# Kernel tuning notes

Hardware: AMD Instinct MI355X
Metric: run time of the kernel (lower is better)

## Reference

```python
import jax, jax.numpy as jnp
import numpy as np

N_LAYERS = 2
D_MODEL = 1024
EXPAND = 2
D_INNER = EXPAND * D_MODEL   # 2048
D_STATE = 16
D_CONV = 4
DT_RANK = (D_MODEL + 15) // 16  # 64
BATCH = 2
SEQ = 1024


def setup_inputs() -> dict:
    key = jax.random.key(0)
    ks = jax.random.split(key, 8)
    x = jax.random.normal(ks[0], (BATCH, SEQ, D_MODEL), jnp.float32)
    in_proj_w = jax.random.normal(ks[1], (N_LAYERS, 2 * D_INNER, D_MODEL), jnp.float32) * 0.02
    conv_w = jax.random.normal(ks[2], (N_LAYERS, D_INNER, 1, D_CONV), jnp.float32) * 0.2
    conv_b = jnp.zeros((N_LAYERS, D_INNER), jnp.float32)
    x_proj_w = jax.random.normal(ks[3], (N_LAYERS, DT_RANK + 2 * D_STATE, D_INNER), jnp.float32) * 0.02
    dt_proj_w = jax.random.normal(ks[4], (N_LAYERS, D_INNER, DT_RANK), jnp.float32) * 0.1
    # softplus(b) ~ 0.01 -> realistic small dt init
    dt_proj_b = jnp.full((N_LAYERS, D_INNER), float(np.log(np.expm1(0.01))), jnp.float32)
    A_log = jnp.tile(jnp.log(jnp.arange(1, D_STATE + 1, dtype=jnp.float32))[None, None, :], (N_LAYERS, D_INNER, 1))
    D = jnp.ones((N_LAYERS, D_INNER), jnp.float32)
    out_proj_w = jax.random.normal(ks[5], (N_LAYERS, D_MODEL, D_INNER), jnp.float32) * 0.02
    return {
        'x': x, 'in_proj_w': in_proj_w, 'conv_w': conv_w, 'conv_b': conv_b,
        'x_proj_w': x_proj_w, 'dt_proj_w': dt_proj_w, 'dt_proj_b': dt_proj_b,
        'A_log': A_log, 'D': D, 'out_proj_w': out_proj_w,
    }


def _mamba_block(x, W_in, w_c, b_c, W_x, W_dt, b_dt, A_log, Dp, W_out):
    # x: (B, L, d_model)
    xz = jnp.einsum('bld,ed->ble', x, W_in)           # (B, L, 2*d_inner)
    xc, z = jnp.split(xz, 2, axis=-1)
    # causal depthwise conv1d over time
    xc = xc.transpose(0, 2, 1)                         # (B, d_inner, L)
    xc = jax.lax.conv_general_dilated(
        xc, w_c, window_strides=(1,), padding=[(D_CONV - 1, 0)],
        dimension_numbers=('NCH', 'OIH', 'NCH'), feature_group_count=D_INNER,
    ) + b_c[None, :, None]
    u = jax.nn.silu(xc).transpose(0, 2, 1)             # (B, L, d_inner)
    # input-dependent dt, B, C
    x_dbl = jnp.einsum('bld,ed->ble', u, W_x)          # (B, L, dt_rank+2N)
    dt, Bm, Cm = jnp.split(x_dbl, [DT_RANK, DT_RANK + D_STATE], axis=-1)
    delta = jax.nn.softplus(jnp.einsum('blr,dr->bld', dt, W_dt) + b_dt)  # (B, L, d_inner)
    A = -jnp.exp(A_log)                                 # (d_inner, N)
    dA = jnp.exp(jnp.einsum('bld,dn->bldn', delta, A))  # (B, L, d_inner, N)
    dBu = jnp.einsum('bld,bln,bld->bldn', delta, Bm, u) # (B, L, d_inner, N)

    def step(h, inp):
        dA_t, dBu_t, C_t = inp                          # (B,d,N), (B,d,N), (B,N)
        h = dA_t * h + dBu_t
        return h, jnp.einsum('bdn,bn->bd', h, C_t)

    h0 = jnp.zeros((x.shape[0], D_INNER, D_STATE), x.dtype)
    _, ys = jax.lax.scan(step, h0, (dA.transpose(1, 0, 2, 3), dBu.transpose(1, 0, 2, 3), Cm.transpose(1, 0, 2)))
    y = ys.transpose(1, 0, 2) + u * Dp                  # (B, L, d_inner)
    y = y * jax.nn.silu(z)
    return jnp.einsum('bld,od->blo', y, W_out)          # (B, L, d_model)


def _forward(x, in_proj_w, conv_w, conv_b, x_proj_w, dt_proj_w, dt_proj_b, A_log, D, out_proj_w):
    residual = x
    for i in range(N_LAYERS):
        x = _mamba_block(x, in_proj_w[i], conv_w[i], conv_b[i], x_proj_w[i],
                         dt_proj_w[i], dt_proj_b[i], A_log[i], D[i], out_proj_w[i])
    return x + residual


def reference(x, in_proj_w, conv_w, conv_b, x_proj_w, dt_proj_w, dt_proj_b, A_log, D, out_proj_w):
    return _forward(x, in_proj_w, conv_w, conv_b, x_proj_w, dt_proj_w, dt_proj_b, A_log, D, out_proj_w)
```

## Files before the change

### kernel.cpp

```cpp
#include <hip/hip_runtime.h>
#include <hip/hip_bf16.h>

#define NLAYERS 2
#define DMODEL 1024
#define DINNER 2048
#define DSTATE 16
#define DCONV 4
#define DTRANK 64
#define BATCH 2
#define SEQ 1024
#define TOK (BATCH * SEQ)

#define NCHUNK 32
#define CLEN (SEQ / NCHUNK)
#define KSX 16
#define KSO 4

typedef short bf16x8 __attribute__((ext_vector_type(8)));
typedef float f32x4 __attribute__((ext_vector_type(4)));
typedef unsigned short ushort8 __attribute__((ext_vector_type(8)));

__device__ __forceinline__ float softplusf(float x) {
    return (x > 20.f) ? x : log1pf(__expf(x));
}
__device__ __forceinline__ float siluf(float x) {
    return x / (1.f + __expf(-x));
}
__device__ __forceinline__ unsigned short f2bf(float f) {
    union { float f; unsigned int u; } v; v.f = f;
    const unsigned int r = (v.u + 0x7FFFu + ((v.u >> 16) & 1u)) >> 16;
    return (unsigned short)r;
}
__device__ __forceinline__ float bf2f(unsigned short s) {
    union { unsigned int u; float f; } v; v.u = ((unsigned int)s) << 16;
    return v.f;
}

__device__ __forceinline__ void cvt8(const float* __restrict__ in,
                                     unsigned short* __restrict__ out, int i) {
    const float4 a = reinterpret_cast<const float4*>(in)[i * 2 + 0];
    const float4 b = reinterpret_cast<const float4*>(in)[i * 2 + 1];
    ushort4 o0, o1;
    o0.x = f2bf(a.x); o0.y = f2bf(a.y); o0.z = f2bf(a.z); o0.w = f2bf(a.w);
    o1.x = f2bf(b.x); o1.y = f2bf(b.y); o1.z = f2bf(b.z); o1.w = f2bf(b.w);
    reinterpret_cast<ushort4*>(out)[i * 2 + 0] = o0;
    reinterpret_cast<ushort4*>(out)[i * 2 + 1] = o1;
}

#define WI8 1048576
#define WO8 524288
#define WX8 49152
#define WD8 32768
#define AC8 262144
__global__ __launch_bounds__(256)
void cvt_all(const float* __restrict__ wi, const float* __restrict__ wo,
             const float* __restrict__ wx, const float* __restrict__ wd,
             const float* __restrict__ xin,
             unsigned short* __restrict__ wi_bf, unsigned short* __restrict__ wo_bf,
             unsigned short* __restrict__ wx_bf, unsigned short* __restrict__ wd_bf,
             unsigned short* __restrict__ act_bf) {
    int i = blockIdx.x * 256 + threadIdx.x;
    if (i < WI8) { cvt8(wi, wi_bf, i); return; }
    i -= WI8;
    if (i < WO8) { cvt8(wo, wo_bf, i); return; }
    i -= WO8;
    if (i < WX8) { cvt8(wx, wx_bf, i); return; }
    i -= WX8;
    if (i < WD8) { cvt8(wd, wd_bf, i); return; }
    i -= WD8;
    if (i < AC8) { cvt8(xin, act_bf, i); return; }
}

template <int EPI>
__global__ __launch_bounds__(256)
void gemm_bf16(const unsigned short* __restrict__ Ab, int lda,
               const unsigned short* __restrict__ Wb, int ldw,
               void* __restrict__ Cptr, int ldc, int kLen, int Nw,
               size_t cSlice, const float* __restrict__ bias) {
    __shared__ unsigned short As[128 * 32];
    __shared__ unsigned short Bs[128 * 32];
    const int tid = threadIdx.x;
    const int wave = tid >> 6, lane = tid & 63;
    const int wr = wave >> 1, wc = wave & 1;
    const int m0 = blockIdx.y * 128, n0 = blockIdx.x * 128;
    const int kbeg = blockIdx.z * kLen;
    const int r = lane & 15, kq = lane >> 4;

    f32x4 acc[4][4] = {};

    for (int kt = kbeg; kt < kbeg + kLen; kt += 32) {
#pragma unroll
        for (int i = 0; i < 2; ++i) {
            const int chunk = i * 256 + tid;
            const int m = chunk >> 2, kc = chunk & 3;
            __builtin_amdgcn_global_load_lds(
                (const __attribute__((address_space(1))) void*)
                    &Ab[(size_t)(m0 + m) * lda + kt + kc * 8],
                (__attribute__((address_space(3))) void*)&As[chunk * 8], 16, 0, 0);
            const int wrow = min(n0 + m, Nw - 1);
            __builtin_amdgcn_global_load_lds(
                (const __attribute__((address_space(1))) void*)
                    &Wb[(size_t)wrow * ldw + kt + kc * 8],
                (__attribute__((address_space(3))) void*)&Bs[chunk * 8], 16, 0, 0);
        }
        __syncthreads();
        bf16x8 a[4], b[4];
#pragma unroll
        for (int f = 0; f < 4; ++f) {
            a[f] = *reinterpret_cast<const bf16x8*>(&As[(wr * 64 + f * 16 + r) * 32 + kq * 8]);
            b[f] = *reinterpret_cast<const bf16x8*>(&Bs[(wc * 64 + f * 16 + r) * 32 + kq * 8]);
        }
#pragma unroll
        for (int fi = 0; fi < 4; ++fi)
#pragma unroll
            for (int fj = 0; fj < 4; ++fj)
                acc[fi][fj] = __builtin_amdgcn_mfma_f32_16x16x32_bf16(
                    a[fi], b[fj], acc[fi][fj], 0, 0, 0);
        __syncthreads();
    }

    const int cr = lane >> 4, cc = lane & 15;
#pragma unroll
    for (int fi = 0; fi < 4; ++fi)
#pragma unroll
        for (int fj = 0; fj < 4; ++fj)
#pragma unroll
            for (int p = 0; p < 4; ++p) {
                const int m = m0 + wr * 64 + fi * 16 + cr * 4 + p;
                const int n = n0 + wc * 64 + fj * 16 + cc;
                const float v = acc[fi][fj][p];
                if (EPI == 0) {
                    if (n < Nw)
                        ((float*)Cptr)[(size_t)blockIdx.z * cSlice +
                                       (size_t)m * ldc + n] = v;
                } else if (EPI == 3) {
                    ((unsigned short*)Cptr)[(size_t)blockIdx.z * cSlice +
                                            (size_t)m * ldc + n] = f2bf(v);
                } else {
                    ((unsigned short*)Cptr)[(size_t)m * ldc + n] =
                        f2bf(softplusf(v + bias[n]));
                }
            }
}

__global__ __launch_bounds__(256)
void conv_silu8(const unsigned short* __restrict__ xz_bf,
                const float* __restrict__ cw,
                const float* __restrict__ cb,
                unsigned short* __restrict__ u_bf) {
    const int gid = blockIdx.x * 256 + threadIdx.x;
    const int d8 = gid & 255;
    const int t = gid >> 8;
    const int l = t & (SEQ - 1);
    const int d0 = d8 * 8;

    float cwv[8][4];
#pragma unroll
    for (int j = 0; j < 8; ++j) {
        const float4 c = *reinterpret_cast<const float4*>(&cw[(d0 + j) * DCONV]);
        cwv[j][0] = c.x; cwv[j][1] = c.y; cwv[j][2] = c.z; cwv[j][3] = c.w;
    }
    float acc[8];
    {
        const float4 b0 = *reinterpret_cast<const float4*>(&cb[d0]);
        const float4 b1 = *reinterpret_cast<const float4*>(&cb[d0 + 4]);
        acc[0] = b0.x; acc[1] = b0.y; acc[2] = b0.z; acc[3] = b0.w;
        acc[4] = b1.x; acc[5] = b1.y; acc[6] = b1.z; acc[7] = b1.w;
    }
#pragma unroll
    for (int k = 0; k < DCONV; ++k) {
        const int li = l - (DCONV - 1) + k;
        if (li >= 0) {
            const ushort8 v = *reinterpret_cast<const ushort8*>(
                &xz_bf[(size_t)(t - (DCONV - 1) + k) * 4096 + d0]);
#pragma unroll
            for (int j = 0; j < 8; ++j)
                acc[j] = fmaf(cwv[j][k], bf2f(v[j]), acc[j]);
        }
    }
    ushort8 o;
#pragma unroll
    for (int j = 0; j < 8; ++j) o[j] = f2bf(siluf(acc[j]));
    *reinterpret_cast<ushort8*>(&u_bf[(size_t)t * DINNER + d0]) = o;
}

__global__ __launch_bounds__(256)
void reduce_x(const float* __restrict__ part, float* __restrict__ xdbl,
              unsigned short* __restrict__ dt_bf) {
    const int i = blockIdx.x * 256 + threadIdx.x;
    if (i >= TOK * 96) return;
    float s = 0.f;
#pragma unroll
    for (int k = 0; k < KSX; ++k) s += part[(size_t)k * (TOK * 96) + i];
    xdbl[i] = s;
    const int t = i / 96, c = i - t * 96;
    if (c < DTRANK) dt_bf[t * DTRANK + c] = f2bf(s);
}

template <int MODE>
__global__ __launch_bounds__(256)
void reduce_out(const unsigned short* __restrict__ part,
                const float* __restrict__ resid, void* __restrict__ outp) {
    const int i = blockIdx.x * 256 + threadIdx.x;
    if (i >= TOK * DMODEL / 4) return;
    float s[4] = {0.f, 0.f, 0.f, 0.f};
#pragma unroll
    for (int k = 0; k < KSO; ++k) {
        const ushort4 p = reinterpret_cast<const ushort4*>(
            &part[(size_t)k * (TOK * DMODEL)])[i];
        s[0] += bf2f(p.x); s[1] += bf2f(p.y); s[2] += bf2f(p.z); s[3] += bf2f(p.w);
    }
    if (MODE == 0) {
        ushort4 o;
        o.x = f2bf(s[0]); o.y = f2bf(s[1]); o.z = f2bf(s[2]); o.w = f2bf(s[3]);
        reinterpret_cast<ushort4*>(outp)[i] = o;
    } else {
        const float4 rr = reinterpret_cast<const float4*>(resid)[i];
        float4 o;
        o.x = s[0] + rr.x; o.y = s[1] + rr.y; o.z = s[2] + rr.z; o.w = s[3] + rr.w;
        reinterpret_cast<float4*>(outp)[i] = o;
    }
}

__device__ __forceinline__ void load_b16(const float* __restrict__ p, float* B) {
    const float4* bp = reinterpret_cast<const float4*>(p);
    const float4 b0 = bp[0], b1 = bp[1], b2 = bp[2], b3 = bp[3];
    B[0] = b0.x; B[1] = b0.y; B[2] = b0.z; B[3] = b0.w;
    B[4] = b1.x; B[5] = b1.y; B[6] = b1.z; B[7] = b1.w;
    B[8] = b2.x; B[9] = b2.y; B[10] = b2.z; B[11] = b2.w;
    B[12] = b3.x; B[13] = b3.y; B[14] = b3.z; B[15] = b3.w;
}

__global__ __launch_bounds__(256)
void scan_partial(const unsigned short* __restrict__ delta_bf,
                  const unsigned short* __restrict__ u_bf,
                  const float* __restrict__ xdbl,
                  const float* __restrict__ A_log,
                  float* __restrict__ hbuf,
                  float* __restrict__ Pbuf) {
    const int b = blockIdx.y / NCHUNK;
    const int c = blockIdx.y % NCHUNK;
    const int d = blockIdx.x * 256 + threadIdx.x;
    const int t0 = b * SEQ + c * CLEN;

    float A_dn[16];
    load_b16(&A_log[d * DSTATE], A_dn);
#pragma unroll
    for (int n = 0; n < 16; ++n) A_dn[n] = -__expf(A_dn[n]);

    float h[16], P[16];
#pragma unroll
    for (int n = 0; n < 16; ++n) { h[n] = 0.f; P[n] = 1.f; }

    float dltA, uvA, BA[16];
    float dltB, uvB, BB[16];
    dltA = bf2f(delta_bf[(size_t)t0 * DINNER + d]);
    uvA = bf2f(u_bf[(size_t)t0 * DINNER + d]);
    load_b16(&xdbl[(size_t)t0 * 96 + DTRANK], BA);

#define PSTEP(dlt_, uv_, Bc_)                              \
    {                                                      \
        const float du = (dlt_) * (uv_);                   \
        _Pragma("unroll")                                  \
        for (int n = 0; n < 16; ++n) {                     \
            const float dA = __expf((dlt_) * A_dn[n]);     \
            h[n] = fmaf(dA, h[n], du * Bc_[n]);            \
            P[n] *= dA;                                    \
        }                                                  \
    }

    for (int l = 0; l < CLEN; l += 2) {
        const int t = t0 + l;
        dltB = bf2f(delta_bf[(size_t)(t + 1) * DINNER + d]);
        uvB = bf2f(u_bf[(size_t)(t + 1) * DINNER + d]);
        load_b16(&xdbl[(size_t)(t + 1) * 96 + DTRANK], BB);
        PSTEP(dltA, uvA, BA);
        if (l + 2 < CLEN) {
            dltA = bf2f(delta_bf[(size_t)(t + 2) * DINNER + d]);
            uvA = bf2f(u_bf[(size_t)(t + 2) * DINNER + d]);
            load_b16(&xdbl[(size_t)(t + 2) * 96 + DTRANK], BA);
        }
        PSTEP(dltB, uvB, BB);
    }
#undef PSTEP

    float* hp = &hbuf[((size_t)(b * NCHUNK + c) * DINNER + d) * DSTATE];
    float* Pp = &Pbuf[((size_t)(b * NCHUNK + c) * DINNER + d) * DSTATE];
#pragma unroll
    for (int q = 0; q < 4; ++q) {
        reinterpret_cast<float4*>(hp)[q] = make_float4(h[q*4], h[q*4+1], h[q*4+2], h[q*4+3]);
        reinterpret_cast<float4*>(Pp)[q] = make_float4(P[q*4], P[q*4+1], P[q*4+2], P[q*4+3]);
    }
}

__global__ __launch_bounds__(256)
void scan_combine(float* __restrict__ hbuf, const float* __restrict__ Pbuf) {
    const int gid = blockIdx.x * 256 + threadIdx.x;
    const int b = gid / (DINNER * DSTATE);
    const int dn = gid - b * (DINNER * DSTATE);
    const size_t base = (size_t)b * NCHUNK * DINNER * DSTATE + dn;
    float hi = 0.f;
#pragma unroll
    for (int c = 0; c < NCHUNK; ++c) {
        const size_t idx = base + (size_t)c * (DINNER * DSTATE);
        const float hl = hbuf[idx];
        const float Pc = Pbuf[idx];
        hbuf[idx] = hi;
        hi = fmaf(Pc, hi, hl);
    }
}

__global__ __launch_bounds__(256)
void scan_final(const unsigned short* __restrict__ delta_bf,
                const unsigned short* __restrict__ u_bf,
                const float* __restrict__ xdbl,
                const unsigned short* __restrict__ xz_bf,
                const float* __restrict__ A_log,
                const float* __restrict__ Dp,
                const float* __restrict__ hbuf,
                unsigned short* __restrict__ yout) {
    const int b = blockIdx.y / NCHUNK;
    const int c = blockIdx.y % NCHUNK;
    const int d = blockIdx.x * 256 + threadIdx.x;
    const int t0 = b * SEQ + c * CLEN;

    float A_dn[16];
    load_b16(&A_log[d * DSTATE], A_dn);
#pragma unroll
    for (int n = 0; n < 16; ++n) A_dn[n] = -__expf(A_dn[n]);
    const float Dd = Dp[d];

    float h[16];
    load_b16(&hbuf[((size_t)(b * NCHUNK + c) * DINNER + d) * DSTATE], h);

    float dltA, uvA, BA[16], CA[16];
    float dltB, uvB, BB[16], CB[16];
    dltA = bf2f(delta_bf[(size_t)t0 * DINNER + d]);
    uvA = bf2f(u_bf[(size_t)t0 * DINNER + d]);
    load_b16(&xdbl[(size_t)t0 * 96 + DTRANK], BA);
    load_b16(&xdbl[(size_t)t0 * 96 + DTRANK + DSTATE], CA);

#define FSTEP(t_, dlt_, uv_, Bc_, Cc_)                          \
    {                                                           \
        const float du = (dlt_) * (uv_);                        \
        _Pragma("unroll")                                       \
        for (int n = 0; n < 16; ++n) {                          \
            const float dA = __expf((dlt_) * A_dn[n]);          \
            h[n] = fmaf(dA, h[n], du * Bc_[n]);                 \
        }                                                       \
        float s0 = 0.f, s1 = 0.f, s2 = 0.f, s3 = 0.f;           \
        _Pragma("unroll")                                       \
        for (int q = 0; q < 4; ++q) {                           \
            s0 = fmaf(h[q*4+0], Cc_[q*4+0], s0);                \
            s1 = fmaf(h[q*4+1], Cc_[q*4+1], s1);                \
            s2 = fmaf(h[q*4+2], Cc_[q*4+2], s2);                \
            s3 = fmaf(h[q*4+3], Cc_[q*4+3], s3);                \
        }                                                       \
        const float zv = bf2f(xz_bf[(size_t)(t_) * 4096 + 2048 + d]); \
        const float y = (s0 + s1) + (s2 + s3) + (uv_) * Dd;     \
        yout[(size_t)(t_) * DINNER + d] = f2bf(y * siluf(zv));  \
    }

    for (int l = 0; l < CLEN; l += 2) {
        const int t = t0 + l;
        dltB = bf2f(delta_bf[(size_t)(t + 1) * DINNER + d]);
        uvB = bf2f(u_bf[(size_t)(t + 1) * DINNER + d]);
        load_b16(&xdbl[(size_t)(t + 1) * 96 + DTRANK], BB);
        load_b16(&xdbl[(size_t)(t + 1) * 96 + DTRANK + DSTATE], CB);
        FSTEP(t, dltA, uvA, BA, CA);
        if (l + 2 < CLEN) {
            dltA = bf2f(delta_bf[(size_t)(t + 2) * DINNER + d]);
            uvA = bf2f(u_bf[(size_t)(t + 2) * DINNER + d]);
            load_b16(&xdbl[(size_t)(t + 2) * 96 + DTRANK], BA);
            load_b16(&xdbl[(size_t)(t + 2) * 96 + DTRANK + DSTATE], CA);
        }
        FSTEP(t + 1, dltB, uvB, BB, CB);
    }
#undef FSTEP
}

extern "C" void kernel_launch(void* const* d_in, const int* in_sizes, int n_in,
                              void* d_out, int out_size, void* d_ws, size_t ws_size,
                              hipStream_t stream) {
    const float* x          = (const float*)d_in[0];
    const float* in_proj_w  = (const float*)d_in[1];
    const float* conv_w     = (const float*)d_in[2];
    const float* conv_b     = (const float*)d_in[3];
    const float* x_proj_w   = (const float*)d_in[4];
    const float* dt_proj_w  = (const float*)d_in[5];
    const float* dt_proj_b  = (const float*)d_in[6];
    const float* A_log      = (const float*)d_in[7];
    const float* Dp         = (const float*)d_in[8];
    const float* out_proj_w = (const float*)d_in[9];
    float* out = (float*)d_out;

    float* ws = (float*)d_ws;
    float* hbuf  = ws;
    float* Pbuf  = hbuf  + 2097152;
    float* xpart = Pbuf  + 2097152;
    float* xdbl  = xpart + 3145728;
    unsigned short* opart  = (unsigned short*)(xdbl + 196608);
    unsigned short* wi_bf  = opart + 8388608;
    unsigned short* wo_bf  = wi_bf + 8388608;
    unsigned short* wx_bf  = wo_bf + 4194304;
    unsigned short* wd_bf  = wx_bf + 393216;
    unsigned short* xz_bf  = wd_bf + 262144;
    unsigned short* u_bf   = xz_bf + 8388608;
    unsigned short* dlt_bf = u_bf  + 4194304;
    unsigned short* act_bf = dlt_bf + 4194304;
    unsigned short* y_bf   = act_bf + 2097152;
    unsigned short* dt_bf  = y_bf  + 4194304;

    cvt_all<<<(WI8 + WO8 + WX8 + WD8 + AC8 + 255) / 256, 256, 0, stream>>>(
        in_proj_w, out_proj_w, x_proj_w, dt_proj_w, x,
        wi_bf, wo_bf, wx_bf, wd_bf, act_bf);

    for (int layer = 0; layer < NLAYERS; ++layer) {
        const unsigned short* Wi = wi_bf + (size_t)layer * (2 * DINNER) * DMODEL;
        const unsigned short* Wo = wo_bf + (size_t)layer * DMODEL * DINNER;
        const unsigned short* Wx = wx_bf + (size_t)layer * 96 * DINNER;
        const unsigned short* Wd = wd_bf + (size_t)layer * DINNER * DTRANK;
        const float* cw = conv_w    + (size_t)layer * DINNER * DCONV;
        const float* cb = conv_b    + (size_t)layer * DINNER;
        const float* bd = dt_proj_b + (size_t)layer * DINNER;
        const float* Al = A_log     + (size_t)layer * DINNER * DSTATE;
        const float* Dl = Dp        + (size_t)layer * DINNER;

        {
            dim3 grid(4096 / 128, TOK / 128, 1);
            gemm_bf16<3><<<grid, 256, 0, stream>>>(act_bf, DMODEL, Wi, DMODEL,
                                                   xz_bf, 2 * DINNER, DMODEL,
                                                   2 * DINNER, 0, nullptr);
        }
        conv_silu8<<<(TOK * 256) / 256, 256, 0, stream>>>(xz_bf, cw, cb, u_bf);
        {
            dim3 grid(1, TOK / 128, KSX);
            gemm_bf16<0><<<grid, 256, 0, stream>>>(u_bf, DINNER, Wx, DINNER,
                                                   xpart, 96, DINNER / KSX, 96,
                                                   (size_t)TOK * 96, nullptr);
            reduce_x<<<(TOK * 96 + 255) / 256, 256, 0, stream>>>(xpart, xdbl, dt_bf);
        }
        {
            dim3 grid(DINNER / 128, TOK / 128, 1);
            gemm_bf16<4><<<grid, 256, 0, stream>>>(dt_bf, DTRANK, Wd, DTRANK,
                                                   dlt_bf, DINNER, DTRANK, DINNER,
                                                   0, bd);
        }
        {
            dim3 gridA(DINNER / 256, BATCH * NCHUNK);
            scan_partial<<<gridA, 256, 0, stream>>>(dlt_bf, u_bf, xdbl, Al,
                                                    hbuf, Pbuf);
            scan_combine<<<(BATCH * DINNER * DSTATE) / 256, 256, 0, stream>>>(hbuf, Pbuf);
            scan_final<<<gridA, 256, 0, stream>>>(dlt_bf, u_bf, xdbl, xz_bf,
                                                  Al, Dl, hbuf, y_bf);
        }
        {
            dim3 grid(DMODEL / 128, TOK / 128, KSO);
            gemm_bf16<3><<<grid, 256, 0, stream>>>(y_bf, DINNER, Wo, DINNER,
                                                   opart, DMODEL, DINNER / KSO,
                                                   DMODEL, (size_t)TOK * DMODEL,
                                                   nullptr);
            const int nred = TOK * DMODEL / 4;
            if (layer == NLAYERS - 1) {
                reduce_out<1><<<(nred + 255) / 256, 256, 0, stream>>>(opart, x, out);
            } else {
                reduce_out<0><<<(nred + 255) / 256, 256, 0, stream>>>(opart, nullptr,
                                                                      act_bf);
            }
        }
    }
}
```

Baseline: 348.7 us.

## Double-buffer GEMM LDS staging and store scan chunk states in bf16

The GEMM now keeps two LDS buffers and issues the next k-tile's global-to-LDS loads before computing on the current tile. It replaces __syncthreads with explicit waitcnt and barriers so memory latency overlaps the MFMA work. Separately, the per-chunk scan state h and decay product P are written, combined and read as bf16 instead of fp32, halving that traffic. The bf16 state adds rounding error to the carried scan state, and the doubled LDS use may lower occupancy.

```diff
diff --git a/kernel.cpp b/kernel.cpp
--- a/kernel.cpp
+++ b/kernel.cpp
@@ -77,38 +77,60 @@
                const unsigned short* __restrict__ Wb, int ldw,
                void* __restrict__ Cptr, int ldc, int kLen, int Nw,
                size_t cSlice, const float* __restrict__ bias) {
-    __shared__ unsigned short As[128 * 32];
-    __shared__ unsigned short Bs[128 * 32];
+    __shared__ unsigned short As[2][128 * 32];
+    __shared__ unsigned short Bs[2][128 * 32];
     const int tid = threadIdx.x;
     const int wave = tid >> 6, lane = tid & 63;
     const int wr = wave >> 1, wc = wave & 1;
     const int m0 = blockIdx.y * 128, n0 = blockIdx.x * 128;
     const int kbeg = blockIdx.z * kLen;
     const int r = lane & 15, kq = lane >> 4;
+    const int nt = kLen >> 5;
+
+    const int ch0 = tid, ch1 = 256 + tid;
+    const int sm0 = ch0 >> 2, sk0 = (ch0 & 3) * 8;
+    const int sm1 = ch1 >> 2, sk1 = (ch1 & 3) * 8;
+    const int wrow0 = min(n0 + sm0, Nw - 1);
+    const int wrow1 = min(n0 + sm1, Nw - 1);
+
+    auto stage = [&](int buf, int kt) {
+        __builtin_amdgcn_global_load_lds(
+            (const __attribute__((address_space(1))) void*)
+                &Ab[(size_t)(m0 + sm0) * lda + kt + sk0],
+            (__attribute__((address_space(3))) void*)&As[buf][ch0 * 8], 16, 0, 0);
+        __builtin_amdgcn_global_load_lds(
+            (const __attribute__((address_space(1))) void*)
+                &Wb[(size_t)wrow0 * ldw + kt + sk0],
+            (__attribute__((address_space(3))) void*)&Bs[buf][ch0 * 8], 16, 0, 0);
+        __builtin_amdgcn_global_load_lds(
+            (const __attribute__((address_space(1))) void*)
+                &Ab[(size_t)(m0 + sm1) * lda + kt + sk1],
+            (__attribute__((address_space(3))) void*)&As[buf][ch1 * 8], 16, 0, 0);
+        __builtin_amdgcn_global_load_lds(
+            (const __attribute__((address_space(1))) void*)
+                &Wb[(size_t)wrow1 * ldw + kt + sk1],
+            (__attribute__((address_space(3))) void*)&Bs[buf][ch1 * 8], 16, 0, 0);
+    };
 
     f32x4 acc[4][4] = {};
-
-    for (int kt = kbeg; kt < kbeg + kLen; kt += 32) {
-#pragma unroll
-        for (int i = 0; i < 2; ++i) {
-            const int chunk = i * 256 + tid;
-            const int m = chunk >> 2, kc = chunk & 3;
-            __builtin_amdgcn_global_load_lds(
-                (const __attribute__((address_space(1))) void*)
-                    &Ab[(size_t)(m0 + m) * lda + kt + kc * 8],
-                (__attribute__((address_space(3))) void*)&As[chunk * 8], 16, 0, 0);
-            const int wrow = min(n0 + m, Nw - 1);
-            __builtin_amdgcn_global_load_lds(
-                (const __attribute__((address_space(1))) void*)
-                    &Wb[(size_t)wrow * ldw + kt + kc * 8],
-                (__attribute__((address_space(3))) void*)&Bs[chunk * 8], 16, 0, 0);
-        }
-        __syncthreads();
+    stage(0, kbeg);
+    for (int t = 0; t < nt; ++t) {
+        const int cur = t & 1;
+        if (t + 1 < nt) {
+            stage(cur ^ 1, kbeg + (t + 1) * 32);
+            asm volatile("s_waitcnt vmcnt(4)" ::: "memory");
+        } else {
+            asm volatile("s_waitcnt vmcnt(0)" ::: "memory");
+        }
+        __builtin_amdgcn_s_barrier();
+        __builtin_amdgcn_sched_barrier(0);
         bf16x8 a[4], b[4];
 #pragma unroll
         for (int f = 0; f < 4; ++f) {
-            a[f] = *reinterpret_cast<const bf16x8*>(&As[(wr * 64 + f * 16 + r) * 32 + kq * 8]);
-            b[f] = *reinterpret_cast<const bf16x8*>(&Bs[(wc * 64 + f * 16 + r) * 32 + kq * 8]);
+            a[f] = *reinterpret_cast<const bf16x8*>(
+                &As[cur][(wr * 64 + f * 16 + r) * 32 + kq * 8]);
+            b[f] = *reinterpret_cast<const bf16x8*>(
+                &Bs[cur][(wc * 64 + f * 16 + r) * 32 + kq * 8]);
         }
 #pragma unroll
         for (int fi = 0; fi < 4; ++fi)
@@ -116,7 +138,9 @@
             for (int fj = 0; fj < 4; ++fj)
                 acc[fi][fj] = __builtin_amdgcn_mfma_f32_16x16x32_bf16(
                     a[fi], b[fj], acc[fi][fj], 0, 0, 0);
-        __syncthreads();
+        __builtin_amdgcn_sched_barrier(0);
+        asm volatile("s_waitcnt lgkmcnt(0)" ::: "memory");
+        __builtin_amdgcn_s_barrier();
     }
 
     const int cr = lane >> 4, cc = lane & 15;
@@ -230,14 +254,29 @@
     B[8] = b2.x; B[9] = b2.y; B[10] = b2.z; B[11] = b2.w;
     B[12] = b3.x; B[13] = b3.y; B[14] = b3.z; B[15] = b3.w;
 }
+__device__ __forceinline__ void load_bf16x16(const unsigned short* __restrict__ p,
+                                             float* B) {
+    const ushort8 v0 = *reinterpret_cast<const ushort8*>(p);
+    const ushort8 v1 = *reinterpret_cast<const ushort8*>(p + 8);
+#pragma unroll
+    for (int j = 0; j < 8; ++j) { B[j] = bf2f(v0[j]); B[8 + j] = bf2f(v1[j]); }
+}
+__device__ __forceinline__ void store_bf16x16(unsigned short* __restrict__ p,
+                                              const float* B) {
+    ushort8 v0, v1;
+#pragma unroll
+    for (int j = 0; j < 8; ++j) { v0[j] = f2bf(B[j]); v1[j] = f2bf(B[8 + j]); }
+    *reinterpret_cast<ushort8*>(p) = v0;
+    *reinterpret_cast<ushort8*>(p + 8) = v1;
+}
 
 __global__ __launch_bounds__(256)
 void scan_partial(const unsigned short* __restrict__ delta_bf,
                   const unsigned short* __restrict__ u_bf,
                   const float* __restrict__ xdbl,
                   const float* __restrict__ A_log,
-                  float* __restrict__ hbuf,
-                  float* __restrict__ Pbuf) {
+                  unsigned short* __restrict__ hbuf,
+                  unsigned short* __restrict__ Pbuf) {
     const int b = blockIdx.y / NCHUNK;
     const int c = blockIdx.y % NCHUNK;
     const int d = blockIdx.x * 256 + threadIdx.x;
@@ -284,17 +323,14 @@
     }
 #undef PSTEP
 
-    float* hp = &hbuf[((size_t)(b * NCHUNK + c) * DINNER + d) * DSTATE];
-    float* Pp = &Pbuf[((size_t)(b * NCHUNK + c) * DINNER + d) * DSTATE];
-#pragma unroll
-    for (int q = 0; q < 4; ++q) {
-        reinterpret_cast<float4*>(hp)[q] = make_float4(h[q*4], h[q*4+1], h[q*4+2], h[q*4+3]);
-        reinterpret_cast<float4*>(Pp)[q] = make_float4(P[q*4], P[q*4+1], P[q*4+2], P[q*4+3]);
-    }
-}
-
-__global__ __launch_bounds__(256)
-void scan_combine(float* __restrict__ hbuf, const float* __restrict__ Pbuf) {
+    const size_t base = ((size_t)(b * NCHUNK + c) * DINNER + d) * DSTATE;
+    store_bf16x16(&hbuf[base], h);
+    store_bf16x16(&Pbuf[base], P);
+}
+
+__global__ __launch_bounds__(256)
+void scan_combine(unsigned short* __restrict__ hbuf,
+                  const unsigned short* __restrict__ Pbuf) {
     const int gid = blockIdx.x * 256 + threadIdx.x;
     const int b = gid / (DINNER * DSTATE);
     const int dn = gid - b * (DINNER * DSTATE);
@@ -303,9 +339,9 @@
 #pragma unroll
     for (int c = 0; c < NCHUNK; ++c) {
         const size_t idx = base + (size_t)c * (DINNER * DSTATE);
-        const float hl = hbuf[idx];
-        const float Pc = Pbuf[idx];
-        hbuf[idx] = hi;
+        const float hl = bf2f(hbuf[idx]);
+        const float Pc = bf2f(Pbuf[idx]);
+        hbuf[idx] = f2bf(hi);
         hi = fmaf(Pc, hi, hl);
     }
 }
@@ -317,7 +353,7 @@
                 const unsigned short* __restrict__ xz_bf,
                 const float* __restrict__ A_log,
                 const float* __restrict__ Dp,
-                const float* __restrict__ hbuf,
+                const unsigned short* __restrict__ hbuf,
                 unsigned short* __restrict__ yout) {
     const int b = blockIdx.y / NCHUNK;
     const int c = blockIdx.y % NCHUNK;
@@ -331,7 +367,7 @@
     const float Dd = Dp[d];
 
     float h[16];
-    load_b16(&hbuf[((size_t)(b * NCHUNK + c) * DINNER + d) * DSTATE], h);
+    load_bf16x16(&hbuf[((size_t)(b * NCHUNK + c) * DINNER + d) * DSTATE], h);
 
     float dltA, uvA, BA[16], CA[16];
     float dltB, uvB, BB[16], CB[16];
@@ -395,11 +431,12 @@
     float* out = (float*)d_out;
 
     float* ws = (float*)d_ws;
-    float* hbuf  = ws;
-    float* Pbuf  = hbuf  + 2097152;
-    float* xpart = Pbuf  + 2097152;
+    float* xpart = ws;
     float* xdbl  = xpart + 3145728;
-    unsigned short* opart  = (unsigned short*)(xdbl + 196608);
+    unsigned short* us = (unsigned short*)(xdbl + 196608);
+    unsigned short* hbuf   = us;
+    unsigned short* Pbuf   = hbuf + 2097152;
+    unsigned short* opart  = Pbuf + 2097152;
     unsigned short* wi_bf  = opart + 8388608;
     unsigned short* wo_bf  = wi_bf + 8388608;
     unsigned short* wx_bf  = wo_bf + 4194304;
```

After: 325.0 us. -6.8%, faster.
